# Kernel optimization log

Measured on AMD Instinct MI355X. Metric: run time of the kernel, lower is better.

Reference implementation:

```python
import jax, jax.numpy as jnp
import numpy as np
import math

B, T, D, H = 64, 256, 512, 1024


def setup_inputs() -> dict:
    key = jax.random.key(0)
    ks = jax.random.split(key, 11)
    stdv = 1.0 / math.sqrt(H)

    def u(k, shape):
        return jax.random.uniform(k, shape, jnp.float32, -stdv, stdv)

    return {
        "x": jax.random.normal(ks[0], (B, T, D), jnp.float32),
        "h0": jax.random.normal(ks[1], (B, H), jnp.float32),
        "ctx": jax.random.normal(ks[2], (B, H), jnp.float32),
        "Wi": u(ks[3], (3 * H, D)), "bi": u(ks[4], (3 * H,)),
        "Wh": u(ks[5], (2 * H, H)), "bh": u(ks[6], (2 * H,)),
        "Wp": u(ks[7], (3 * H, H)), "bp": u(ks[8], (3 * H,)),
        "Wc": u(ks[9], (H, H)),     "bc": u(ks[10], (H,)),
    }


def reference(x, h0, ctx, Wi, bi, Wh, bh, Wp, bp, Wc, bc):
    # Input gates for all timesteps in one batched GEMM: [B,T,3H] -> time-major [T,B,3H]
    ig_all = jnp.einsum("btd,gd->tbg", x, Wi) + bi
    # Peephole gate depends only on ctx -> compute once. [B,3H]
    p_r, p_i, p_n = jnp.split(ctx @ Wp.T + bp, 3, axis=-1)

    def step(h, ig):
        i_r, i_i, i_n = jnp.split(ig, 3, axis=-1)
        h_r, h_i = jnp.split(h @ Wh.T + bh, 2, axis=-1)
        resetgate = jax.nn.sigmoid(i_r + h_r + p_r)
        inputgate = jax.nn.sigmoid(i_i + h_i + p_i)
        h_n = (resetgate * h) @ Wc.T + bc
        newgate = jnp.tanh(i_n + h_n + p_n)
        hy = h + inputgate * (newgate - h)
        return hy, hy

    hT, ys = jax.lax.scan(step, h0, ig_all)  # ys: [T,B,H]
    output = jnp.transpose(ys, (1, 0, 2))    # [B,T,H]
    return output, hT
```

## Files before the change

### kernel.cpp

```cpp
#include <hip/hip_runtime.h>
#include <hip/hip_bf16.h>
#include <math.h>

#define Bz 64
#define Tz 256
#define Dz 512
#define Hz 1024
#define G3 3072
#define NBK 64

typedef short bf16x8 __attribute__((ext_vector_type(8)));
typedef float f32x4 __attribute__((ext_vector_type(4)));

__device__ __forceinline__ float sigm(float x){ return 1.0f/(1.0f+expf(-x)); }

__device__ __forceinline__ unsigned short f2b(float f){
  union{float f;unsigned u;}v; v.f=f;
  unsigned r = v.u + 0x7FFFu + ((v.u>>16)&1u);
  return (unsigned short)(r>>16);
}
__device__ __forceinline__ float b2f(unsigned short s){
  union{unsigned u;float f;}v; v.u = ((unsigned)s)<<16; return v.f;
}
__device__ __forceinline__ unsigned pk2(float a, float b){
  return (unsigned)f2b(a) | ((unsigned)f2b(b)<<16);
}

__device__ __forceinline__ unsigned long long cld64(const void* p){
  return __hip_atomic_load((const unsigned long long*)p, __ATOMIC_RELAXED, __HIP_MEMORY_SCOPE_AGENT);
}
__device__ __forceinline__ void cst64(void* p, unsigned long long v){
  __hip_atomic_store((unsigned long long*)p, v, __ATOMIC_RELAXED, __HIP_MEMORY_SCOPE_AGENT);
}
__device__ __forceinline__ float2 cldf2(const float* p){
  union { unsigned long long u; float2 f; } U; U.u = cld64(p); return U.f;
}
__device__ __forceinline__ void cstf2(float* p, float a, float b){
  union { unsigned long long u; float2 f; } U; U.f = make_float2(a,b); cst64(p, U.u);
}
__device__ __forceinline__ int cld32(const int* p){
  return __hip_atomic_load(p, __ATOMIC_RELAXED, __HIP_MEMORY_SCOPE_AGENT);
}
__device__ __forceinline__ void cst32(int* p, int v){
  __hip_atomic_store(p, v, __ATOMIC_RELAXED, __HIP_MEMORY_SCOPE_AGENT);
}

#define KCHUNK 128
#define LDA 132
template<int COLS, int KDIM>
__device__ __forceinline__ void gemm_core(const float* __restrict__ Abase, int rowStride,
                                          const float* __restrict__ W,
                                          int jc0, int b, int tid,
                                          float* __restrict__ acc, float* __restrict__ lds)
{
#pragma unroll
  for (int c=0;c<COLS;c++) acc[c]=0.0f;
  constexpr int C4 = KCHUNK/4;
  for (int kb=0; kb<KDIM; kb+=KCHUNK) {
    __syncthreads();
    for (int i = tid; i < Bz*C4; i += 256) {
      int r  = i / C4;
      int c4 = i % C4;
      float4 v = *(const float4*)(Abase + (size_t)r*rowStride + kb + c4*4);
      *(float4*)(lds + r*LDA + c4*4) = v;
    }
    __syncthreads();
    const float* arow  = lds + b*LDA;
    const float* wbase = W + (size_t)jc0*KDIM + kb;
    for (int k=0;k<KCHUNK;k+=4) {
      float4 a = *(const float4*)(arow + k);
#pragma unroll
      for (int c=0;c<COLS;c++) {
        float4 w = *(const float4*)(wbase + (size_t)c*KDIM + k);
        acc[c] = fmaf(a.x,w.x,fmaf(a.y,w.y,fmaf(a.z,w.z,fmaf(a.w,w.w,acc[c]))));
      }
    }
  }
}

__global__ __launch_bounds__(256)
void kP(const float* __restrict__ ctx, const float* __restrict__ Wp,
        const float* __restrict__ bp, const float* __restrict__ bh,
        const float* __restrict__ bc, const float* __restrict__ bi,
        float* __restrict__ pT)
{
  __shared__ float lds[Bz*LDA];
  int tid=threadIdx.x; int b=tid&63;
  int wv=__builtin_amdgcn_readfirstlane(tid>>6);
  int jc0 = blockIdx.x*16 + wv*4;
  float acc[4];
  gemm_core<4, Hz>(ctx, Hz, Wp, jc0, b, tid, acc, lds);
#pragma unroll
  for(int c=0;c<4;c++){
    int j=jc0+c;
    float v = acc[c] + bp[j] + bi[j] + (j < 2*Hz ? bh[j] : bc[j-2*Hz]);
    pT[(size_t)j*64 + b] = v;
  }
}

__global__ __launch_bounds__(256)
void kI(const float* __restrict__ h0, float* __restrict__ hF, unsigned short* __restrict__ hB)
{
  int b = blockIdx.x;
  int j = threadIdx.x*4;
  float4 v = *(const float4*)(h0 + (size_t)b*Hz + j);
  *(float4*)(hF + ((size_t)(j>>2)*64 + b)*4) = v;
  unsigned long long pk = (unsigned long long)pk2(v.x,v.y)
                        | ((unsigned long long)pk2(v.z,v.w) << 32);
  *(unsigned long long*)(hB + (size_t)b*Hz + j) = pk;
}

__global__ __launch_bounds__(1024)
void kAm(const float* __restrict__ x, const float* __restrict__ Wi,
         const float* __restrict__ pT, unsigned short* __restrict__ igT)
{
  __shared__ unsigned short wiF[4*16*64*8];
  __shared__ unsigned short xs[64*528];
  __shared__ unsigned short igs[64*64];
  const int tid = threadIdx.x;
  const int lane = tid & 63;
  const int w = __builtin_amdgcn_readfirstlane(tid >> 6);
  const int j0 = blockIdx.x * 64;
  const int t0 = blockIdx.y * 16;
  const int mt = w >> 2, nt = w & 3;
  const int bb = nt*16 + (lane & 15);
  const int q  = lane >> 4;
  const int jl = mt*16 + q*4;

  for (int idx = tid; idx < 4096; idx += 1024) {
    int mt2 = idx >> 10;
    int ks = (idx >> 6) & 15;
    int ln = idx & 63;
    int j = j0 + mt2*16 + (ln & 15);
    int k = ks*32 + (ln >> 4)*8;
    const float* s = Wi + (size_t)j*Dz + k;
    unsigned short* d = wiF + (size_t)idx*8;
#pragma unroll
    for (int qq=0;qq<8;qq++) d[qq] = f2b(s[qq]);
  }
  float pv[4];
#pragma unroll
  for (int r=0;r<4;r++) pv[r] = pT[(size_t)(j0+jl+r)*64 + bb];

  for (int it=0; it<16; it++) {
    int t = t0 + it;
    __syncthreads();
    for (int i = tid; i < 64*32; i += 1024) {
      int b = i >> 5, c = i & 31;
      const float* s = x + ((size_t)b*Tz + t)*Dz + c*16;
      unsigned* d = (unsigned*)(xs + (size_t)b*528 + c*16);
      float4 v0 = *(const float4*)(s);
      float4 v1 = *(const float4*)(s+4);
      float4 v2 = *(const float4*)(s+8);
      float4 v3 = *(const float4*)(s+12);
      d[0]=pk2(v0.x,v0.y); d[1]=pk2(v0.z,v0.w);
      d[2]=pk2(v1.x,v1.y); d[3]=pk2(v1.z,v1.w);
      d[4]=pk2(v2.x,v2.y); d[5]=pk2(v2.z,v2.w);
      d[6]=pk2(v3.x,v3.y); d[7]=pk2(v3.z,v3.w);
    }
    __syncthreads();
    f32x4 acc = {0.f,0.f,0.f,0.f};
    const unsigned short* bsrc = xs + (size_t)bb*528 + q*8;
#pragma unroll
    for (int ks=0; ks<16; ks++) {
      bf16x8 a = *(const bf16x8*)(wiF + ((size_t)(mt*16+ks)*64 + lane)*8);
      bf16x8 b = *(const bf16x8*)(bsrc + ks*32);
      acc = __builtin_amdgcn_mfma_f32_16x16x32_bf16(a, b, acc, 0, 0, 0);
    }
#pragma unroll
    for (int r=0;r<4;r++) igs[(size_t)(jl+r)*64 + bb] = f2b(acc[r] + pv[r]);
    __syncthreads();
    if (tid < 512) {
      int j = tid >> 3, seg = tid & 7;
      *(uint4*)(igT + ((size_t)t*G3 + j0 + j)*64 + seg*8) =
        *(const uint4*)(igs + (size_t)j*64 + seg*8);
    }
  }
}

__global__ __launch_bounds__(1024)
void krec(const float* __restrict__ Wh, const float* __restrict__ Wc,
          const unsigned short* __restrict__ igT,
          float* __restrict__ hF0, float* __restrict__ hF1,
          unsigned short* __restrict__ hB0, unsigned short* __restrict__ hB1,
          unsigned short* __restrict__ rhB, float* __restrict__ iT,
          float* __restrict__ out, int* canP, int* canH)
{
  __shared__ unsigned short whF[2*32*64*8];
  __shared__ unsigned short wcF[32*64*8];
  __shared__ float red[32*64*4];
  const int tid = threadIdx.x;
  const int lane = tid & 63;
  const int w = __builtin_amdgcn_readfirstlane(tid >> 6);
  const int n = blockIdx.x;

  for (int idx = tid; idx < 4096; idx += 1024) {
    int mt = idx >> 11;
    int ks = (idx >> 6) & 31;
    int ln = idx & 63;
    int j = n*32 + mt*16 + (ln & 15);
    int k = ks*32 + (ln >> 4)*8;
    const float* s = Wh + (size_t)j*Hz + k;
    unsigned short* d = whF + (size_t)idx*8;
#pragma unroll
    for (int qq=0;qq<8;qq++) d[qq] = f2b(s[qq]);
  }
  for (int idx = tid; idx < 2048; idx += 1024) {
    int ks = (idx >> 6) & 31;
    int ln = idx & 63;
    int j = n*16 + (ln & 15);
    int k = ks*32 + (ln >> 4)*8;
    const float* s = Wc + (size_t)j*Hz + k;
    unsigned short* d = wcF + (size_t)idx*8;
#pragma unroll
    for (int qq=0;qq<8;qq++) d[qq] = f2b(s[qq]);
  }

  const int nt = w & 3;
  const int kh = w >> 2;
  const int bb = nt*16 + (lane & 15);
  const int q  = lane >> 4;

  for (int t=0;t<Tz;t++) {
    const unsigned short* igt = igT + (size_t)t*G3*64;
    const unsigned short* hBr = (t&1) ? hB1 : hB0;
    unsigned short*       hBw = (t&1) ? hB0 : hB1;
    const float*          hFr = (t&1) ? hF1 : hF0;
    float*                hFw = (t&1) ? hF0 : hF1;
    {
      float igv[4];
      if (w < 8) {
        int jg = n*32 + (w>>2)*16 + q*4;
#pragma unroll
        for (int r=0;r<4;r++) igv[r] = b2f(igt[(size_t)(jg+r)*64 + bb]);
      }
      {
        const int* p = canH + kh*16 + (lane & 15);
        while (!__all(cld32(p) >= t)) __builtin_amdgcn_s_sleep(2);
        asm volatile("" ::: "memory");
      }
      bf16x8 bfr[8];
      {
        unsigned voff = (unsigned)(bb*2048 + q*16 + kh*512);
        asm volatile(
          "global_load_dwordx4 %0, %8, %9 sc0 sc1\n\t"
          "global_load_dwordx4 %1, %8, %9 offset:64 sc0 sc1\n\t"
          "global_load_dwordx4 %2, %8, %9 offset:128 sc0 sc1\n\t"
          "global_load_dwordx4 %3, %8, %9 offset:192 sc0 sc1\n\t"
          "global_load_dwordx4 %4, %8, %9 offset:256 sc0 sc1\n\t"
          "global_load_dwordx4 %5, %8, %9 offset:320 sc0 sc1\n\t"
          "global_load_dwordx4 %6, %8, %9 offset:384 sc0 sc1\n\t"
          "global_load_dwordx4 %7, %8, %9 offset:448 sc0 sc1\n\t"
          "s_waitcnt vmcnt(0)"
          : "=v"(bfr[0]), "=v"(bfr[1]), "=v"(bfr[2]), "=v"(bfr[3]),
            "=v"(bfr[4]), "=v"(bfr[5]), "=v"(bfr[6]), "=v"(bfr[7])
          : "v"(voff), "s"(hBr)
          : "memory");
      }
      f32x4 acc0 = {0.f,0.f,0.f,0.f}, acc1 = {0.f,0.f,0.f,0.f};
      const unsigned short* a0 = whF + ((size_t)(kh*8)*64 + lane)*8;
      const unsigned short* a1 = whF + ((size_t)(32 + kh*8)*64 + lane)*8;
#pragma unroll
      for (int ks=0; ks<8; ks++) {
        bf16x8 A0 = *(const bf16x8*)(a0 + (size_t)ks*512);
        bf16x8 A1 = *(const bf16x8*)(a1 + (size_t)ks*512);
        acc0 = __builtin_amdgcn_mfma_f32_16x16x32_bf16(A0, bfr[ks], acc0, 0, 0, 0);
        acc1 = __builtin_amdgcn_mfma_f32_16x16x32_bf16(A1, bfr[ks], acc1, 0, 0, 0);
      }
      *(f32x4*)(red + ((size_t)((kh*4+nt)*2+0)*64 + lane)*4) = acc0;
      *(f32x4*)(red + ((size_t)((kh*4+nt)*2+1)*64 + lane)*4) = acc1;
      __syncthreads();
      if (w < 8) {
        int emt = w >> 2, ent = w & 3;
        int jg = n*32 + emt*16 + q*4;
        f32x4 s = {0.f,0.f,0.f,0.f};
#pragma unroll
        for (int kk=0; kk<4; kk++) {
          f32x4 v = *(const f32x4*)(red + ((size_t)((kk*4+ent)*2+emt)*64 + lane)*4);
          s[0]+=v[0]; s[1]+=v[1]; s[2]+=v[2]; s[3]+=v[3];
        }
        if (n < 32) {
          const float* hp = hFr + ((size_t)(jg>>2)*64 + bb)*4;
          float2 a01 = cldf2(hp), a23 = cldf2(hp+2);
          float hv[4] = {a01.x, a01.y, a23.x, a23.y};
          unsigned long long pk = 0;
#pragma unroll
          for (int r=0;r<4;r++) {
            float g = sigm(s[r] + igv[r]);
            pk |= (unsigned long long)f2b(g * hv[r]) << (16*r);
          }
          cst64(rhB + (size_t)bb*Hz + jg, pk);
        } else {
          float g0 = sigm(s[0] + igv[0]);
          float g1 = sigm(s[1] + igv[1]);
          float g2 = sigm(s[2] + igv[2]);
          float g3 = sigm(s[3] + igv[3]);
          float* ip = iT + ((size_t)((jg-1024)>>2)*64 + bb)*4;
          cstf2(ip, g0, g1); cstf2(ip+2, g2, g3);
        }
      }
      __syncthreads();
      if (tid == 0) cst32(canP + n, t+1);
    }
    {
      float igv[4];
      if (w < 4) {
        int jn = n*16 + q*4;
#pragma unroll
        for (int r=0;r<4;r++) igv[r] = b2f(igt[(size_t)(2048+jn+r)*64 + bb]);
      }
      {
        int pi = kh*8 + (lane & 7);
        if (w == 0 && lane >= 56) pi = 32 + (n >> 1);
        const int* p = canP + pi;
        while (!__all(cld32(p) >= t+1)) __builtin_amdgcn_s_sleep(2);
        asm volatile("" ::: "memory");
      }
      bf16x8 bfr[8];
      {
        unsigned voff = (unsigned)(bb*2048 + q*16 + kh*512);
        asm volatile(
          "global_load_dwordx4 %0, %8, %9 sc0 sc1\n\t"
          "global_load_dwordx4 %1, %8, %9 offset:64 sc0 sc1\n\t"
          "global_load_dwordx4 %2, %8, %9 offset:128 sc0 sc1\n\t"
          "global_load_dwordx4 %3, %8, %9 offset:192 sc0 sc1\n\t"
          "global_load_dwordx4 %4, %8, %9 offset:256 sc0 sc1\n\t"
          "global_load_dwordx4 %5, %8, %9 offset:320 sc0 sc1\n\t"
          "global_load_dwordx4 %6, %8, %9 offset:384 sc0 sc1\n\t"
          "global_load_dwordx4 %7, %8, %9 offset:448 sc0 sc1\n\t"
          "s_waitcnt vmcnt(0)"
          : "=v"(bfr[0]), "=v"(bfr[1]), "=v"(bfr[2]), "=v"(bfr[3]),
            "=v"(bfr[4]), "=v"(bfr[5]), "=v"(bfr[6]), "=v"(bfr[7])
          : "v"(voff), "s"(rhB)
          : "memory");
      }
      f32x4 acc = {0.f,0.f,0.f,0.f};
#pragma unroll
      for (int ks=0; ks<8; ks++) {
        bf16x8 a = *(const bf16x8*)(wcF + ((size_t)(kh*8+ks)*64 + lane)*8);
        acc = __builtin_amdgcn_mfma_f32_16x16x32_bf16(a, bfr[ks], acc, 0, 0, 0);
      }
      *(f32x4*)(red + ((size_t)w*64 + lane)*4) = acc;
      __syncthreads();
      if (w < 4) {
        f32x4 s0 = *(const f32x4*)(red + ((size_t)w*64+lane)*4);
        f32x4 s1 = *(const f32x4*)(red + ((size_t)(w+4)*64+lane)*4);
        f32x4 s2 = *(const f32x4*)(red + ((size_t)(w+8)*64+lane)*4);
        f32x4 s3 = *(const f32x4*)(red + ((size_t)(w+12)*64+lane)*4);
        int jn = n*16 + q*4;
        const float* hp = hFr + ((size_t)(jn>>2)*64 + bb)*4;
        float2 a01 = cldf2(hp), a23 = cldf2(hp+2);
        float hv[4] = {a01.x, a01.y, a23.x, a23.y};
        const float* ip = iT + ((size_t)(jn>>2)*64 + bb)*4;
        float2 b01 = cldf2(ip), b23 = cldf2(ip+2);
        float iv[4] = {b01.x, b01.y, b23.x, b23.y};
        float hy4[4];
        unsigned long long pk = 0;
#pragma unroll
        for (int r=0;r<4;r++) {
          float g  = s0[r]+s1[r]+s2[r]+s3[r] + igv[r];
          float ng = tanhf(g);
          float hy = hv[r] + iv[r]*(ng - hv[r]);
          hy4[r] = hy;
          pk |= (unsigned long long)f2b(hy) << (16*r);
        }
        float* hpw = hFw + ((size_t)(jn>>2)*64 + bb)*4;
        cstf2(hpw,   hy4[0], hy4[1]);
        cstf2(hpw+2, hy4[2], hy4[3]);
        cst64(hBw + (size_t)bb*Hz + jn, pk);
        float4 ov; ov.x=hy4[0]; ov.y=hy4[1]; ov.z=hy4[2]; ov.w=hy4[3];
        *(float4*)(out + ((size_t)bb*Tz + t)*Hz + jn) = ov;
      }
      __syncthreads();
      if (tid == 0) cst32(canH + n, t+1);
    }
  }
}

__global__ __launch_bounds__(256)
void ktr(const float* __restrict__ hF, float* __restrict__ hN)
{
  int b = blockIdx.x;
  int j = threadIdx.x*4;
  float4 v = *(const float4*)(hF + ((size_t)(j>>2)*64 + b)*4);
  *(float4*)(hN + (size_t)b*Hz + j) = v;
}

extern "C" void kernel_launch(void* const* d_in, const int* in_sizes, int n_in,
                              void* d_out, int out_size, void* d_ws, size_t ws_size,
                              hipStream_t stream)
{
  const float* x   = (const float*)d_in[0];
  const float* h0  = (const float*)d_in[1];
  const float* ctx = (const float*)d_in[2];
  const float* Wi  = (const float*)d_in[3];
  const float* bi  = (const float*)d_in[4];
  const float* Wh  = (const float*)d_in[5];
  const float* bh  = (const float*)d_in[6];
  const float* Wp  = (const float*)d_in[7];
  const float* bp  = (const float*)d_in[8];
  const float* Wc  = (const float*)d_in[9];
  const float* bc  = (const float*)d_in[10];
  float* out = (float*)d_out;

  char* wsp = (char*)d_ws;
  float* pT  = (float*)wsp; wsp += (size_t)G3*64*sizeof(float);
  float* hF0 = (float*)wsp; wsp += (size_t)Hz*64*sizeof(float);
  float* hF1 = (float*)wsp; wsp += (size_t)Hz*64*sizeof(float);
  float* iT  = (float*)wsp; wsp += (size_t)Hz*64*sizeof(float);
  unsigned short* hB0 = (unsigned short*)wsp; wsp += (size_t)Bz*Hz*2;
  unsigned short* hB1 = (unsigned short*)wsp; wsp += (size_t)Bz*Hz*2;
  unsigned short* rhB = (unsigned short*)wsp; wsp += (size_t)Bz*Hz*2;
  int* canP = (int*)wsp; wsp += 512;
  int* canH = canP + 64;
  unsigned short* igT = (unsigned short*)wsp;

  hipMemsetAsync(canP, 0, 512, stream);
  kP  <<<dim3(G3/16),   256,  0, stream>>>(ctx, Wp, bp, bh, bc, bi, pT);
  kI  <<<dim3(64),      256,  0, stream>>>(h0, hF0, hB0);
  kAm <<<dim3(48,16),   1024, 0, stream>>>(x, Wi, pT, igT);
  krec<<<dim3(NBK),     1024, 0, stream>>>(Wh, Wc, igT, hF0, hF1, hB0, hB1, rhB, iT, out, canP, canH);
  ktr <<<dim3(64),      256,  0, stream>>>(hF0, out + (size_t)Bz*Tz*Hz);
}
```

Before: 3.972 ms.

## Replace per-block flags with per-wave readiness flags in recurrent kernel

Turns the block-wide cross-block flags (canP, canH) into per-wave flags. Each finishing wave publishes its own counter after a vmcnt wait, so the trailing __syncthreads and single-thread flag store at the end of each phase go away. Consumers now poll only the specific wave flags they depend on. The loads of h and the input gate are hoisted ahead of the MFMA work, and the shared reduction buffer is split into two so the phases do not overwrite each other without a barrier. This should shorten the critical path per timestep, at the cost of more flag polling and more subtle memory-ordering correctness.

```diff
diff --git a/kernel.cpp b/kernel.cpp
--- a/kernel.cpp
+++ b/kernel.cpp
@@ -188,7 +188,8 @@
 {
   __shared__ unsigned short whF[2*32*64*8];
   __shared__ unsigned short wcF[32*64*8];
-  __shared__ float red[32*64*4];
+  __shared__ float red1[32*64*4];
+  __shared__ float red2[16*64*4];
   const int tid = threadIdx.x;
   const int lane = tid & 63;
   const int w = __builtin_amdgcn_readfirstlane(tid >> 6);
@@ -228,16 +229,25 @@
     const float*          hFr = (t&1) ? hF1 : hF0;
     float*                hFw = (t&1) ? hF0 : hF1;
     {
-      float igv[4];
+      float igv[4], hv[4];
       if (w < 8) {
-        int jg = n*32 + (w>>2)*16 + q*4;
+        int jg = n*32 + kh*16 + q*4;
 #pragma unroll
         for (int r=0;r<4;r++) igv[r] = b2f(igt[(size_t)(jg+r)*64 + bb]);
       }
       {
-        const int* p = canH + kh*16 + (lane & 15);
+        const int* p = canH + (kh*16 + (lane & 15))*4 + nt;
         while (!__all(cld32(p) >= t)) __builtin_amdgcn_s_sleep(2);
         asm volatile("" ::: "memory");
+      }
+      if (w < 8 && n < 32) {
+        const int* ph = canH + (n*2 + kh)*4 + nt;
+        while (cld32(ph) < t) __builtin_amdgcn_s_sleep(2);
+        asm volatile("" ::: "memory");
+        int jg = n*32 + kh*16 + q*4;
+        const float* hp = hFr + ((size_t)(jg>>2)*64 + bb)*4;
+        float2 a01 = cldf2(hp), a23 = cldf2(hp+2);
+        hv[0]=a01.x; hv[1]=a01.y; hv[2]=a23.x; hv[3]=a23.y;
       }
       bf16x8 bfr[8];
       {
@@ -267,22 +277,18 @@
         acc0 = __builtin_amdgcn_mfma_f32_16x16x32_bf16(A0, bfr[ks], acc0, 0, 0, 0);
         acc1 = __builtin_amdgcn_mfma_f32_16x16x32_bf16(A1, bfr[ks], acc1, 0, 0, 0);
       }
-      *(f32x4*)(red + ((size_t)((kh*4+nt)*2+0)*64 + lane)*4) = acc0;
-      *(f32x4*)(red + ((size_t)((kh*4+nt)*2+1)*64 + lane)*4) = acc1;
+      *(f32x4*)(red1 + ((size_t)((kh*4+nt)*2+0)*64 + lane)*4) = acc0;
+      *(f32x4*)(red1 + ((size_t)((kh*4+nt)*2+1)*64 + lane)*4) = acc1;
       __syncthreads();
       if (w < 8) {
-        int emt = w >> 2, ent = w & 3;
-        int jg = n*32 + emt*16 + q*4;
+        int jg = n*32 + kh*16 + q*4;
         f32x4 s = {0.f,0.f,0.f,0.f};
 #pragma unroll
         for (int kk=0; kk<4; kk++) {
-          f32x4 v = *(const f32x4*)(red + ((size_t)((kk*4+ent)*2+emt)*64 + lane)*4);
+          f32x4 v = *(const f32x4*)(red1 + ((size_t)((kk*4+nt)*2+kh)*64 + lane)*4);
           s[0]+=v[0]; s[1]+=v[1]; s[2]+=v[2]; s[3]+=v[3];
         }
         if (n < 32) {
-          const float* hp = hFr + ((size_t)(jg>>2)*64 + bb)*4;
-          float2 a01 = cldf2(hp), a23 = cldf2(hp+2);
-          float hv[4] = {a01.x, a01.y, a23.x, a23.y};
           unsigned long long pk = 0;
 #pragma unroll
           for (int r=0;r<4;r++) {
@@ -298,23 +304,33 @@
           float* ip = iT + ((size_t)((jg-1024)>>2)*64 + bb)*4;
           cstf2(ip, g0, g1); cstf2(ip+2, g2, g3);
         }
-      }
-      __syncthreads();
-      if (tid == 0) cst32(canP + n, t+1);
+        asm volatile("s_waitcnt vmcnt(0)" ::: "memory");
+        cst32(canP + n*8 + w, t+1);
+      }
     }
     {
-      float igv[4];
+      float igv[4], hv[4], iv[4];
       if (w < 4) {
         int jn = n*16 + q*4;
 #pragma unroll
         for (int r=0;r<4;r++) igv[r] = b2f(igt[(size_t)(2048+jn+r)*64 + bb]);
+        const float* hp = hFr + ((size_t)(jn>>2)*64 + bb)*4;
+        float2 a01 = cldf2(hp), a23 = cldf2(hp+2);
+        hv[0]=a01.x; hv[1]=a01.y; hv[2]=a23.x; hv[3]=a23.y;
       }
       {
-        int pi = kh*8 + (lane & 7);
-        if (w == 0 && lane >= 56) pi = 32 + (n >> 1);
-        const int* p = canP + pi;
+        const int* p = canP + (kh*8 + ((lane & 15) >> 1))*8 + ((lane & 1) << 2) + nt;
         while (!__all(cld32(p) >= t+1)) __builtin_amdgcn_s_sleep(2);
         asm volatile("" ::: "memory");
+      }
+      if (w < 4) {
+        const int* pi = canP + (32 + (n >> 1))*8 + ((n & 1) << 2) + w;
+        while (cld32(pi) < t+1) __builtin_amdgcn_s_sleep(2);
+        asm volatile("" ::: "memory");
+        int jn = n*16 + q*4;
+        const float* ip = iT + ((size_t)(jn>>2)*64 + bb)*4;
+        float2 b01 = cldf2(ip), b23 = cldf2(ip+2);
+        iv[0]=b01.x; iv[1]=b01.y; iv[2]=b23.x; iv[3]=b23.y;
       }
       bf16x8 bfr[8];
       {
@@ -340,20 +356,14 @@
         bf16x8 a = *(const bf16x8*)(wcF + ((size_t)(kh*8+ks)*64 + lane)*8);
         acc = __builtin_amdgcn_mfma_f32_16x16x32_bf16(a, bfr[ks], acc, 0, 0, 0);
       }
-      *(f32x4*)(red + ((size_t)w*64 + lane)*4) = acc;
+      *(f32x4*)(red2 + ((size_t)w*64 + lane)*4) = acc;
       __syncthreads();
       if (w < 4) {
-        f32x4 s0 = *(const f32x4*)(red + ((size_t)w*64+lane)*4);
-        f32x4 s1 = *(const f32x4*)(red + ((size_t)(w+4)*64+lane)*4);
-        f32x4 s2 = *(const f32x4*)(red + ((size_t)(w+8)*64+lane)*4);
-        f32x4 s3 = *(const f32x4*)(red + ((size_t)(w+12)*64+lane)*4);
+        f32x4 s0 = *(const f32x4*)(red2 + ((size_t)w*64+lane)*4);
+        f32x4 s1 = *(const f32x4*)(red2 + ((size_t)(w+4)*64+lane)*4);
+        f32x4 s2 = *(const f32x4*)(red2 + ((size_t)(w+8)*64+lane)*4);
+        f32x4 s3 = *(const f32x4*)(red2 + ((size_t)(w+12)*64+lane)*4);
         int jn = n*16 + q*4;
-        const float* hp = hFr + ((size_t)(jn>>2)*64 + bb)*4;
-        float2 a01 = cldf2(hp), a23 = cldf2(hp+2);
-        float hv[4] = {a01.x, a01.y, a23.x, a23.y};
-        const float* ip = iT + ((size_t)(jn>>2)*64 + bb)*4;
-        float2 b01 = cldf2(ip), b23 = cldf2(ip+2);
-        float iv[4] = {b01.x, b01.y, b23.x, b23.y};
         float hy4[4];
         unsigned long long pk = 0;
 #pragma unroll
@@ -370,9 +380,9 @@
         cst64(hBw + (size_t)bb*Hz + jn, pk);
         float4 ov; ov.x=hy4[0]; ov.y=hy4[1]; ov.z=hy4[2]; ov.w=hy4[3];
         *(float4*)(out + ((size_t)bb*Tz + t)*Hz + jn) = ov;
-      }
-      __syncthreads();
-      if (tid == 0) cst32(canH + n, t+1);
+        asm volatile("s_waitcnt vmcnt(0)" ::: "memory");
+        cst32(canH + n*4 + w, t+1);
+      }
     }
   }
 }
@@ -411,11 +421,11 @@
   unsigned short* hB0 = (unsigned short*)wsp; wsp += (size_t)Bz*Hz*2;
   unsigned short* hB1 = (unsigned short*)wsp; wsp += (size_t)Bz*Hz*2;
   unsigned short* rhB = (unsigned short*)wsp; wsp += (size_t)Bz*Hz*2;
-  int* canP = (int*)wsp; wsp += 512;
-  int* canH = canP + 64;
+  int* canP = (int*)wsp; wsp += 4096;
+  int* canH = canP + 512;
   unsigned short* igT = (unsigned short*)wsp;
 
-  hipMemsetAsync(canP, 0, 512, stream);
+  hipMemsetAsync(canP, 0, 4096, stream);
   kP  <<<dim3(G3/16),   256,  0, stream>>>(ctx, Wp, bp, bh, bc, bi, pT);
   kI  <<<dim3(64),      256,  0, stream>>>(h0, hF0, hB0);
   kAm <<<dim3(48,16),   1024, 0, stream>>>(x, Wi, pT, igT);
```

After: 4.614 ms. 1.16x slower.
